# Kernel optimization log

Measured on AMD Instinct MI355X. Metric: run time of the kernel, lower is better.

## Reference

```python
import jax, jax.numpy as jnp
import numpy as np

EMBED_DIM = 1024
HEAD_SIZE = 64
BATCH = 8
SEQ = 2048


def setup_inputs() -> dict:
    key = jax.random.key(0)
    k1, k2, k3, k4 = jax.random.split(key, 4)
    x = jax.random.normal(k1, (BATCH, SEQ, EMBED_DIM), dtype=jnp.float32)
    # Dense(use_bias=False) kernels: [in, out]
    scale = 1.0 / np.sqrt(EMBED_DIM)
    Wq = jax.random.normal(k2, (EMBED_DIM, HEAD_SIZE), dtype=jnp.float32) * scale
    Wk = jax.random.normal(k3, (EMBED_DIM, HEAD_SIZE), dtype=jnp.float32) * scale
    Wv = jax.random.normal(k4, (EMBED_DIM, HEAD_SIZE), dtype=jnp.float32) * scale
    return {"x": x, "Wq": Wq, "Wk": Wk, "Wv": Wv}


def reference(x, Wq, Wk, Wv):
    B, S, E = x.shape
    q = jnp.einsum("bse,eh->bsh", x, Wq)
    k = jnp.einsum("bse,eh->bsh", x, Wk)
    v = jnp.einsum("bse,eh->bsh", x, Wv)
    # scores scaled by embedding_dim**-0.5 (as in the original code)
    w = jnp.einsum("bqh,bkh->bqk", q, k) * (E ** -0.5)
    causal = jnp.tril(jnp.ones((S, S), dtype=bool))  # True on/below diag
    w = jnp.where(causal, w, -jnp.inf)
    w = jax.nn.softmax(w, axis=-1)
    # dropout is identity at inference
    return jnp.einsum("bqk,bkh->bqh", w, v)
```

## Files before the change

### kernel.cpp

```cpp
#include <hip/hip_runtime.h>
#include <hip/hip_bf16.h>


#define BATCH 8
#define SEQ   2048
#define EMB   1024
#define HD    64
#define ROWS  (BATCH*SEQ)
#define NTOT  192

typedef __attribute__((ext_vector_type(8))) short short8;
typedef __attribute__((ext_vector_type(4))) float floatx4;

static __device__ __forceinline__ short f2bf(float f) {
  union { __hip_bfloat16 h; short s; } u;
  u.h = __float2bfloat16(f);
  return u.s;
}

__global__ __launch_bounds__(256) void wt_kernel(
    const float* __restrict__ Wq, const float* __restrict__ Wk,
    const float* __restrict__ Wv, short* __restrict__ Wt) {
  const int i = blockIdx.x * 256 + threadIdx.x;
  const int np = i % NTOT;
  const int c4 = i / NTOT;
  const float* __restrict__ W = (np < 64) ? Wq : ((np < 128) ? Wk : Wv);
  const int n = np & 63;
  short4 o;
  o.x = f2bf(W[(c4 * 4 + 0) * HD + n]);
  o.y = f2bf(W[(c4 * 4 + 1) * HD + n]);
  o.z = f2bf(W[(c4 * 4 + 2) * HD + n]);
  o.w = f2bf(W[(c4 * 4 + 3) * HD + n]);
  *(short4*)(Wt + (size_t)np * EMB + c4 * 4) = o;
}

__global__ __launch_bounds__(256, 2) void proj_kernel(
    const float* __restrict__ x, const short* __restrict__ Wt,
    short* __restrict__ qb, short* __restrict__ kb, short* __restrict__ vtb) {
  __shared__ floatx4 red[2][2][12][64];

  const int t = threadIdx.x, lane = t & 63, w = t >> 6;
  const int lo = lane & 15, quad = lane >> 4;
  const int m0 = blockIdx.x * 32;
  const int k0 = w * 256;

  const float* __restrict__ xr0 = x + (size_t)(m0 + lo) * EMB + k0 + quad * 8;
  const float* __restrict__ xr1 = xr0 + (size_t)16 * EMB;
  const short* __restrict__ wr = Wt + (size_t)lo * EMB + k0 + quad * 8;

  floatx4 acc0[12], acc1[12];
#pragma unroll
  for (int nt = 0; nt < 12; ++nt) {
    acc0[nt] = (floatx4){0.f, 0.f, 0.f, 0.f};
    acc1[nt] = (floatx4){0.f, 0.f, 0.f, 0.f};
  }

  float4 a[2][4];
  a[0][0] = *(const float4*)(xr0);
  a[0][1] = *(const float4*)(xr0 + 4);
  a[0][2] = *(const float4*)(xr1);
  a[0][3] = *(const float4*)(xr1 + 4);

  for (int ks = 0; ks < 8; ++ks) {
    const int cur = ks & 1, nxt = cur ^ 1;
    short8 bfr[12];
#pragma unroll
    for (int nt = 0; nt < 12; ++nt)
      bfr[nt] = *(const short8*)(wr + ks * 32 + (size_t)nt * 16 * EMB);
    if (ks < 7) {
      const int off = (ks + 1) * 32;
      a[nxt][0] = *(const float4*)(xr0 + off);
      a[nxt][1] = *(const float4*)(xr0 + off + 4);
      a[nxt][2] = *(const float4*)(xr1 + off);
      a[nxt][3] = *(const float4*)(xr1 + off + 4);
    }
    short8 af0, af1;
    af0[0] = f2bf(a[cur][0].x); af0[1] = f2bf(a[cur][0].y);
    af0[2] = f2bf(a[cur][0].z); af0[3] = f2bf(a[cur][0].w);
    af0[4] = f2bf(a[cur][1].x); af0[5] = f2bf(a[cur][1].y);
    af0[6] = f2bf(a[cur][1].z); af0[7] = f2bf(a[cur][1].w);
    af1[0] = f2bf(a[cur][2].x); af1[1] = f2bf(a[cur][2].y);
    af1[2] = f2bf(a[cur][2].z); af1[3] = f2bf(a[cur][2].w);
    af1[4] = f2bf(a[cur][3].x); af1[5] = f2bf(a[cur][3].y);
    af1[6] = f2bf(a[cur][3].z); af1[7] = f2bf(a[cur][3].w);
#pragma unroll
    for (int nt = 0; nt < 12; ++nt) {
      acc0[nt] = __builtin_amdgcn_mfma_f32_16x16x32_bf16(af0, bfr[nt], acc0[nt], 0, 0, 0);
      acc1[nt] = __builtin_amdgcn_mfma_f32_16x16x32_bf16(af1, bfr[nt], acc1[nt], 0, 0, 0);
    }
  }

  if (w >= 2) {
#pragma unroll
    for (int nt = 0; nt < 12; ++nt) {
      red[w - 2][0][nt][lane] = acc0[nt];
      red[w - 2][1][nt][lane] = acc1[nt];
    }
  }
  __syncthreads();
  if (w < 2) {
#pragma unroll
    for (int nt = 0; nt < 12; ++nt) {
      acc0[nt] += red[w][0][nt][lane];
      acc1[nt] += red[w][1][nt][lane];
    }
  }
  __syncthreads();
  if (w == 0) {
#pragma unroll
    for (int nt = 0; nt < 12; ++nt) red[0][0][nt][lane] = acc1[nt];
  } else if (w == 1) {
#pragma unroll
    for (int nt = 0; nt < 12; ++nt) red[0][1][nt][lane] = acc0[nt];
  }
  __syncthreads();

  if (w < 2) {
    floatx4 fin[12];
#pragma unroll
    for (int nt = 0; nt < 12; ++nt)
      fin[nt] = (w == 0) ? (acc0[nt] + red[0][1][nt][lane])
                         : (acc1[nt] + red[0][0][nt][lane]);
    const int mf = w;
    const int bb = m0 >> 11;
    const int rowb = m0 + mf * 16 + quad * 4;
#pragma unroll
    for (int nt = 0; nt < 4; ++nt) {
#pragma unroll
      for (int r = 0; r < 4; ++r)
        qb[(size_t)(rowb + r) * HD + nt * 16 + lo] = f2bf(fin[nt][r] * 0.03125f);
    }
#pragma unroll
    for (int nt = 4; nt < 8; ++nt) {
#pragma unroll
      for (int r = 0; r < 4; ++r)
        kb[(size_t)(rowb + r) * HD + (nt - 4) * 16 + lo] = f2bf(fin[nt][r]);
    }
#pragma unroll
    for (int nt = 8; nt < 12; ++nt) {
      const int col = (nt - 8) * 16 + lo;
      const int s0 = (m0 & (SEQ - 1)) + mf * 16 + quad * 4;
      short4 sv = make_short4(f2bf(fin[nt][0]), f2bf(fin[nt][1]),
                              f2bf(fin[nt][2]), f2bf(fin[nt][3]));
      *(short4*)(vtb + ((size_t)bb * HD + col) * SEQ + s0) = sv;
    }
  }
}

#define KSTR 72
#define PSTR 40

__global__ __launch_bounds__(256, 2) void attn_kernel(
    const short* __restrict__ qb, const short* __restrict__ kb,
    const short* __restrict__ vtb, float* __restrict__ out) {
  __shared__ __align__(16) short Ks[2][64 * KSTR];
  __shared__ __align__(16) short Vs[2][64 * KSTR];
  __shared__ __align__(16) short Ps[4][16 * PSTR];
  __shared__ __align__(16) floatx4 Red[2][5][64];

  const int b = blockIdx.y;
  const int bx = blockIdx.x;
  const int qx = (bx & 1) ? (63 - (bx >> 1)) : (bx >> 1);
  const int q0 = qx * 32;
  const int t = threadIdx.x, lane = t & 63, w = t >> 6;
  const int wr = w >> 1, wk = w & 1;
  const int lo = lane & 15, quad = lane >> 4;

  const short* qp = qb + ((size_t)b * SEQ + q0 + wr * 16 + lo) * HD + quad * 8;
  const short8 qf0 = *(const short8*)(qp);
  const short8 qf1 = *(const short8*)(qp + 32);

  const int r0 = t >> 3, c0 = (t & 7) * 8;
  const int r1 = r0 + 32;
  const short* __restrict__ kgb = kb + (size_t)b * SEQ * HD;
  const short* __restrict__ vgb = vtb + (size_t)b * HD * SEQ;

  floatx4 acc[4];
  float lsum[4] = {0.f, 0.f, 0.f, 0.f};
#pragma unroll
  for (int nt = 0; nt < 4; ++nt) acc[nt] = (floatx4){0.f, 0.f, 0.f, 0.f};

  {
    short8 k0v = *(const short8*)(kgb + (size_t)r0 * HD + c0);
    short8 k1v = *(const short8*)(kgb + (size_t)r1 * HD + c0);
    short8 v0v = *(const short8*)(vgb + (size_t)r0 * SEQ + c0);
    short8 v1v = *(const short8*)(vgb + (size_t)r1 * SEQ + c0);
    *(short8*)(&Ks[0][r0 * KSTR + c0]) = k0v;
    *(short8*)(&Ks[0][r1 * KSTR + c0]) = k1v;
    *(short8*)(&Vs[0][r0 * KSTR + c0]) = v0v;
    *(short8*)(&Vs[0][r1 * KSTR + c0]) = v1v;
  }

  const int niter = q0 / 64 + 1;
  for (int it = 0; it < niter; ++it) {
    const int j0 = it * 64;
    const int buf = it & 1;
    __syncthreads();

    short8 kfr[2][2], vfr[4];
#pragma unroll
    for (int n2 = 0; n2 < 2; ++n2) {
      const short* kr = &Ks[buf][(wk * 32 + n2 * 16 + lo) * KSTR + quad * 8];
      kfr[n2][0] = *(const short8*)(kr);
      kfr[n2][1] = *(const short8*)(kr + 32);
    }
#pragma unroll
    for (int nt = 0; nt < 4; ++nt)
      vfr[nt] = *(const short8*)(&Vs[buf][(nt * 16 + lo) * KSTR + wk * 32 + quad * 8]);

    short8 nk0, nk1, nv0, nv1;
    const bool more = (it + 1 < niter);
    if (more) {
      const int jn = j0 + 64;
      nk0 = *(const short8*)(kgb + (size_t)(jn + r0) * HD + c0);
      nk1 = *(const short8*)(kgb + (size_t)(jn + r1) * HD + c0);
      nv0 = *(const short8*)(vgb + (size_t)r0 * SEQ + jn + c0);
      nv1 = *(const short8*)(vgb + (size_t)r1 * SEQ + jn + c0);
    }

    floatx4 s0 = (floatx4){0.f, 0.f, 0.f, 0.f};
    floatx4 s1 = (floatx4){0.f, 0.f, 0.f, 0.f};
    s0 = __builtin_amdgcn_mfma_f32_16x16x32_bf16(qf0, kfr[0][0], s0, 0, 0, 0);
    s0 = __builtin_amdgcn_mfma_f32_16x16x32_bf16(qf1, kfr[0][1], s0, 0, 0, 0);
    s1 = __builtin_amdgcn_mfma_f32_16x16x32_bf16(qf0, kfr[1][0], s1, 0, 0, 0);
    s1 = __builtin_amdgcn_mfma_f32_16x16x32_bf16(qf1, kfr[1][1], s1, 0, 0, 0);

    const bool diag = (j0 + 64 > q0);
    const int rowb = q0 + wr * 16 + quad * 4;
    short* Pw = Ps[w];
#pragma unroll
    for (int r = 0; r < 4; ++r) {
      float e0 = __expf(s0[r]);
      float e1 = __expf(s1[r]);
      if (diag) {
        const int key0 = j0 + wk * 32 + lo;
        e0 = (key0 <= rowb + r) ? e0 : 0.f;
        e1 = (key0 + 16 <= rowb + r) ? e1 : 0.f;
      }
      lsum[r] += e0 + e1;
      Pw[(quad * 4 + r) * PSTR + lo] = f2bf(e0);
      Pw[(quad * 4 + r) * PSTR + 16 + lo] = f2bf(e1);
    }
    const short8 pf = *(const short8*)(&Pw[lo * PSTR + quad * 8]);
#pragma unroll
    for (int nt = 0; nt < 4; ++nt)
      acc[nt] = __builtin_amdgcn_mfma_f32_16x16x32_bf16(pf, vfr[nt], acc[nt], 0, 0, 0);

    if (more) {
      const int nb = buf ^ 1;
      *(short8*)(&Ks[nb][r0 * KSTR + c0]) = nk0;
      *(short8*)(&Ks[nb][r1 * KSTR + c0]) = nk1;
      *(short8*)(&Vs[nb][r0 * KSTR + c0]) = nv0;
      *(short8*)(&Vs[nb][r1 * KSTR + c0]) = nv1;
    }
  }

#pragma unroll
  for (int d = 1; d < 16; d <<= 1) {
#pragma unroll
    for (int r = 0; r < 4; ++r) lsum[r] += __shfl_xor(lsum[r], d);
  }

  if (wk == 1) {
#pragma unroll
    for (int nt = 0; nt < 4; ++nt) Red[wr][nt][lane] = acc[nt];
    Red[wr][4][lane] = (floatx4){lsum[0], lsum[1], lsum[2], lsum[3]};
  }
  __syncthreads();
  if (wk == 0) {
    const floatx4 lp = Red[wr][4][lane];
    const int rowb = q0 + wr * 16 + quad * 4;
#pragma unroll
    for (int nt = 0; nt < 4; ++nt) {
      const floatx4 o = acc[nt] + Red[wr][nt][lane];
#pragma unroll
      for (int r = 0; r < 4; ++r)
        out[((size_t)b * SEQ + rowb + r) * HD + nt * 16 + lo] =
            o[r] / (lsum[r] + lp[r]);
    }
  }
}

extern "C" void kernel_launch(void* const* d_in, const int* in_sizes, int n_in,
                              void* d_out, int out_size, void* d_ws, size_t ws_size,
                              hipStream_t stream) {
  const float* x  = (const float*)d_in[0];
  const float* Wq = (const float*)d_in[1];
  const float* Wk = (const float*)d_in[2];
  const float* Wv = (const float*)d_in[3];
  float* out = (float*)d_out;
  short* ws = (short*)d_ws;
  short* qbp = ws;
  short* kbp = ws + (size_t)ROWS * HD;
  short* vtp = ws + (size_t)2 * ROWS * HD;
  short* Wt  = ws + (size_t)3 * ROWS * HD;

  wt_kernel<<<dim3(NTOT), 256, 0, stream>>>(Wq, Wk, Wv, Wt);
  proj_kernel<<<dim3(ROWS / 32), 256, 0, stream>>>(x, Wt, qbp, kbp, vtp);
  attn_kernel<<<dim3(SEQ / 32, BATCH), 256, 0, stream>>>(qbp, kbp, vtp, out);
}
```

Before: 156.5 us.

## Halve projection row tile and prefetch all x loads up front

The projection kernel now handles 16 rows per block instead of 32, which doubles the grid size. Each wave issues all eight of its x-row loads before the MFMA loop rather than double-buffering them one step at a time. The cross-wave reduction is cut from three barriers to two, and the final writes are split so each of the two surviving waves finalizes half of the 12 output tiles. This targets memory-latency hiding and parallelism on the x stream, which is the dominant read, at the cost of reading Wt twice as often per row and using more registers for the preloaded x.

```diff
diff --git a/kernel.cpp b/kernel.cpp
--- a/kernel.cpp
+++ b/kernel.cpp
@@ -37,112 +37,95 @@
 __global__ __launch_bounds__(256, 2) void proj_kernel(
     const float* __restrict__ x, const short* __restrict__ Wt,
     short* __restrict__ qb, short* __restrict__ kb, short* __restrict__ vtb) {
-  __shared__ floatx4 red[2][2][12][64];
+  __shared__ floatx4 red[2][12][64];
 
   const int t = threadIdx.x, lane = t & 63, w = t >> 6;
   const int lo = lane & 15, quad = lane >> 4;
-  const int m0 = blockIdx.x * 32;
+  const int m0 = blockIdx.x * 16;
   const int k0 = w * 256;
 
-  const float* __restrict__ xr0 = x + (size_t)(m0 + lo) * EMB + k0 + quad * 8;
-  const float* __restrict__ xr1 = xr0 + (size_t)16 * EMB;
+  const float* __restrict__ xr = x + (size_t)(m0 + lo) * EMB + k0 + quad * 8;
   const short* __restrict__ wr = Wt + (size_t)lo * EMB + k0 + quad * 8;
 
-  floatx4 acc0[12], acc1[12];
-#pragma unroll
-  for (int nt = 0; nt < 12; ++nt) {
-    acc0[nt] = (floatx4){0.f, 0.f, 0.f, 0.f};
-    acc1[nt] = (floatx4){0.f, 0.f, 0.f, 0.f};
-  }
-
-  float4 a[2][4];
-  a[0][0] = *(const float4*)(xr0);
-  a[0][1] = *(const float4*)(xr0 + 4);
-  a[0][2] = *(const float4*)(xr1);
-  a[0][3] = *(const float4*)(xr1 + 4);
-
+  floatx4 acc[12];
+#pragma unroll
+  for (int nt = 0; nt < 12; ++nt) acc[nt] = (floatx4){0.f, 0.f, 0.f, 0.f};
+
+  float4 a[8][2];
+#pragma unroll
   for (int ks = 0; ks < 8; ++ks) {
-    const int cur = ks & 1, nxt = cur ^ 1;
+    a[ks][0] = *(const float4*)(xr + ks * 32);
+    a[ks][1] = *(const float4*)(xr + ks * 32 + 4);
+  }
+
+#pragma unroll
+  for (int ks = 0; ks < 8; ++ks) {
     short8 bfr[12];
 #pragma unroll
     for (int nt = 0; nt < 12; ++nt)
       bfr[nt] = *(const short8*)(wr + ks * 32 + (size_t)nt * 16 * EMB);
-    if (ks < 7) {
-      const int off = (ks + 1) * 32;
-      a[nxt][0] = *(const float4*)(xr0 + off);
-      a[nxt][1] = *(const float4*)(xr0 + off + 4);
-      a[nxt][2] = *(const float4*)(xr1 + off);
-      a[nxt][3] = *(const float4*)(xr1 + off + 4);
-    }
-    short8 af0, af1;
-    af0[0] = f2bf(a[cur][0].x); af0[1] = f2bf(a[cur][0].y);
-    af0[2] = f2bf(a[cur][0].z); af0[3] = f2bf(a[cur][0].w);
-    af0[4] = f2bf(a[cur][1].x); af0[5] = f2bf(a[cur][1].y);
-    af0[6] = f2bf(a[cur][1].z); af0[7] = f2bf(a[cur][1].w);
-    af1[0] = f2bf(a[cur][2].x); af1[1] = f2bf(a[cur][2].y);
-    af1[2] = f2bf(a[cur][2].z); af1[3] = f2bf(a[cur][2].w);
-    af1[4] = f2bf(a[cur][3].x); af1[5] = f2bf(a[cur][3].y);
-    af1[6] = f2bf(a[cur][3].z); af1[7] = f2bf(a[cur][3].w);
-#pragma unroll
-    for (int nt = 0; nt < 12; ++nt) {
-      acc0[nt] = __builtin_amdgcn_mfma_f32_16x16x32_bf16(af0, bfr[nt], acc0[nt], 0, 0, 0);
-      acc1[nt] = __builtin_amdgcn_mfma_f32_16x16x32_bf16(af1, bfr[nt], acc1[nt], 0, 0, 0);
-    }
+    short8 af;
+    af[0] = f2bf(a[ks][0].x); af[1] = f2bf(a[ks][0].y);
+    af[2] = f2bf(a[ks][0].z); af[3] = f2bf(a[ks][0].w);
+    af[4] = f2bf(a[ks][1].x); af[5] = f2bf(a[ks][1].y);
+    af[6] = f2bf(a[ks][1].z); af[7] = f2bf(a[ks][1].w);
+#pragma unroll
+    for (int nt = 0; nt < 12; ++nt)
+      acc[nt] = __builtin_amdgcn_mfma_f32_16x16x32_bf16(af, bfr[nt], acc[nt], 0, 0, 0);
   }
 
   if (w >= 2) {
 #pragma unroll
-    for (int nt = 0; nt < 12; ++nt) {
-      red[w - 2][0][nt][lane] = acc0[nt];
-      red[w - 2][1][nt][lane] = acc1[nt];
-    }
+    for (int nt = 0; nt < 12; ++nt) red[w - 2][nt][lane] = acc[nt];
   }
   __syncthreads();
   if (w < 2) {
 #pragma unroll
-    for (int nt = 0; nt < 12; ++nt) {
-      acc0[nt] += red[w][0][nt][lane];
-      acc1[nt] += red[w][1][nt][lane];
+    for (int nt = 0; nt < 12; ++nt) acc[nt] += red[w][nt][lane];
+    if (w == 0) {
+#pragma unroll
+      for (int nt = 6; nt < 12; ++nt) red[0][nt - 6][lane] = acc[nt];
+    } else {
+#pragma unroll
+      for (int nt = 0; nt < 6; ++nt) red[1][nt][lane] = acc[nt];
     }
   }
   __syncthreads();
-  if (w == 0) {
-#pragma unroll
-    for (int nt = 0; nt < 12; ++nt) red[0][0][nt][lane] = acc1[nt];
-  } else if (w == 1) {
-#pragma unroll
-    for (int nt = 0; nt < 12; ++nt) red[0][1][nt][lane] = acc0[nt];
-  }
-  __syncthreads();
 
   if (w < 2) {
-    floatx4 fin[12];
-#pragma unroll
-    for (int nt = 0; nt < 12; ++nt)
-      fin[nt] = (w == 0) ? (acc0[nt] + red[0][1][nt][lane])
-                         : (acc1[nt] + red[0][0][nt][lane]);
-    const int mf = w;
     const int bb = m0 >> 11;
-    const int rowb = m0 + mf * 16 + quad * 4;
-#pragma unroll
-    for (int nt = 0; nt < 4; ++nt) {
-#pragma unroll
-      for (int r = 0; r < 4; ++r)
-        qb[(size_t)(rowb + r) * HD + nt * 16 + lo] = f2bf(fin[nt][r] * 0.03125f);
-    }
-#pragma unroll
-    for (int nt = 4; nt < 8; ++nt) {
-#pragma unroll
-      for (int r = 0; r < 4; ++r)
-        kb[(size_t)(rowb + r) * HD + (nt - 4) * 16 + lo] = f2bf(fin[nt][r]);
-    }
-#pragma unroll
-    for (int nt = 8; nt < 12; ++nt) {
-      const int col = (nt - 8) * 16 + lo;
-      const int s0 = (m0 & (SEQ - 1)) + mf * 16 + quad * 4;
-      short4 sv = make_short4(f2bf(fin[nt][0]), f2bf(fin[nt][1]),
-                              f2bf(fin[nt][2]), f2bf(fin[nt][3]));
-      *(short4*)(vtb + ((size_t)bb * HD + col) * SEQ + s0) = sv;
+    const int s0 = (m0 & (SEQ - 1)) + quad * 4;
+    const int rowb = m0 + quad * 4;
+    if (w == 0) {
+      floatx4 fin[6];
+#pragma unroll
+      for (int nt = 0; nt < 6; ++nt) fin[nt] = acc[nt] + red[1][nt][lane];
+#pragma unroll
+      for (int nt = 0; nt < 4; ++nt)
+#pragma unroll
+        for (int r = 0; r < 4; ++r)
+          qb[(size_t)(rowb + r) * HD + nt * 16 + lo] = f2bf(fin[nt][r] * 0.03125f);
+#pragma unroll
+      for (int nt = 4; nt < 6; ++nt)
+#pragma unroll
+        for (int r = 0; r < 4; ++r)
+          kb[(size_t)(rowb + r) * HD + (nt - 4) * 16 + lo] = f2bf(fin[nt][r]);
+    } else {
+      floatx4 fin[6];
+#pragma unroll
+      for (int nt = 0; nt < 6; ++nt) fin[nt] = acc[nt + 6] + red[0][nt][lane];
+#pragma unroll
+      for (int nt = 0; nt < 2; ++nt)
+#pragma unroll
+        for (int r = 0; r < 4; ++r)
+          kb[(size_t)(rowb + r) * HD + (nt + 2) * 16 + lo] = f2bf(fin[nt][r]);
+#pragma unroll
+      for (int nt = 2; nt < 6; ++nt) {
+        const int col = (nt - 2) * 16 + lo;
+        short4 sv = make_short4(f2bf(fin[nt][0]), f2bf(fin[nt][1]),
+                                f2bf(fin[nt][2]), f2bf(fin[nt][3]));
+        *(short4*)(vtb + ((size_t)bb * HD + col) * SEQ + s0) = sv;
+      }
     }
   }
 }
@@ -296,6 +279,6 @@
   short* Wt  = ws + (size_t)3 * ROWS * HD;
 
   wt_kernel<<<dim3(NTOT), 256, 0, stream>>>(Wq, Wk, Wv, Wt);
-  proj_kernel<<<dim3(ROWS / 32), 256, 0, stream>>>(x, Wt, qbp, kbp, vtp);
+  proj_kernel<<<dim3(ROWS / 16), 256, 0, stream>>>(x, Wt, qbp, kbp, vtp);
   attn_kernel<<<dim3(SEQ / 32, BATCH), 256, 0, stream>>>(qbp, kbp, vtp, out);
 }
```

Result: slower. 175.4 us (+12.1%).
